# Optimization experiments

Hardware: AMD Instinct MI355X
Metric: run time of the kernel (lower is better)

The kernel has to match this reference:

```python
import jax, jax.numpy as jnp
import numpy as np

SIZE_DICT = 512
DIM_DICT = 64
TEMPERATURE = 0.5
EPS = 1e-10


def setup_inputs() -> dict:
    key = jax.random.key(0)
    k1, k2, k3 = jax.random.split(key, 3)
    bs, dz, W, H = 32, 64, 32, 32
    z = jax.random.normal(k1, (bs, dz, W, H), dtype=jnp.float32)
    var_q = jnp.ones((1,), dtype=jnp.float32)
    codebook = jax.random.normal(k2, (SIZE_DICT, DIM_DICT), dtype=jnp.float32)
    gumbel_u = jax.random.uniform(k3, (bs * W * H, SIZE_DICT), dtype=jnp.float32)
    return {"z_from_encoder": z, "var_q": var_q, "codebook": codebook, "gumbel_u": gumbel_u}


def reference(z_from_encoder, var_q, codebook, gumbel_u):
    bs, dz, W, H = z_from_encoder.shape
    # permute to channels-last and flatten: [N, D]
    z_flat = jnp.transpose(z_from_encoder, (0, 2, 3, 1)).reshape(-1, dz)
    # precision with clamping as in torch code
    precision_q = jnp.clip(1.0 / jnp.clip(var_q, 1e-5, None), None, 1e5)  # [1]
    half_prec = 0.5 * precision_q
    # squared euclidean distances to codebook: [N, K]
    dist = (jnp.sum(z_flat ** 2, axis=1, keepdims=True)
            + jnp.sum(codebook ** 2, axis=1)
            - 2.0 * z_flat @ codebook.T)
    logit = -half_prec * dist
    logit = logit - jnp.max(logit, axis=-1, keepdims=True)
    logit = jnp.clip(logit, -50.0, 50.0)
    probabilities = jax.nn.softmax(logit, axis=-1)
    log_probabilities = jax.nn.log_softmax(logit, axis=-1)
    # Gumbel-softmax sampling (training path)
    g = -jnp.log(-jnp.log(gumbel_u + EPS) + EPS)
    encodings = jax.nn.softmax((logit + g) / TEMPERATURE, axis=-1)
    # soft codebook lookup
    z_quantized = (encodings @ codebook).reshape(bs, W, H, dz)
    z_to_decoder = jnp.transpose(z_quantized, (0, 3, 1, 2))  # [bs, D, W, H]
    # discrete KLD term: sum_{n,k} p log p / bs
    kld_discrete = jnp.sum(probabilities * log_probabilities) / bs
    # continuous KLD term: mean over batch of weighted squared error
    kld_continuous = jnp.mean(
        jnp.sum((z_from_encoder - z_to_decoder) ** 2 * half_prec, axis=(1, 2, 3)))
    loss = kld_discrete + kld_continuous
    # perplexity from detached probabilities
    avg_probs = jnp.clip(jnp.mean(jax.lax.stop_gradient(probabilities), axis=0), 1e-10, None)
    perplexity = jnp.exp(-jnp.sum(avg_probs * jnp.log(avg_probs + 1e-10)))
    return z_to_decoder, loss, perplexity
```

## Files before the change

### kernel.cpp

```cpp
#include <hip/hip_runtime.h>


typedef _Float16 half8 __attribute__((ext_vector_type(8)));
typedef float f32x4 __attribute__((ext_vector_type(4)));

#define WS_B1   4096
#define WS_B2   20480
#define WS_PROB 36864
#define WS_LOSS 299008
#define WS_RED  303104
#define WS_NEED 319488

#define SMEM_PRE 24064
#define SMEM_FB  155136

__device__ __forceinline__ float half_prec(const float* var_q) {
  float vq = var_q[0];
  float pq = fminf(1.0f / fmaxf(vq, 1e-5f), 1e5f);
  return 0.5f * pq;
}

__global__ void k_pre(const float* __restrict__ var_q,
                      const float* __restrict__ cb,
                      float* __restrict__ ws, int pre) {
  int t = threadIdx.x, wg = blockIdx.x;
  if (wg == 0) {
    float hp = half_prec(var_q);
    if (t == 0) ws[512] = 0.0f;
    ws[516 + t] = 0.0f;
    const float4* row = (const float4*)(cb + t * 64);
    float s = 0.0f;
    #pragma unroll
    for (int i = 0; i < 16; ++i) {
      float4 v = row[i];
      s += v.x*v.x + v.y*v.y + v.z*v.z + v.w*v.w;
    }
    ws[t] = hp * s;
  }
  if (!pre) return;
  int gid = wg * 512 + t;
  if (gid < 4096) {
    int l = gid & 63, grp = gid >> 6;
    int tt = grp >> 1, kk = grp & 1;
    int cc = l & 15, gg = l >> 4;
    const float* src = cb + (cc*32 + tt)*64 + kk*32 + gg*8;
    float4 v0 = *(const float4*)src;
    float4 v1 = *(const float4*)(src + 4);
    half8 h = { (_Float16)v0.x, (_Float16)v0.y, (_Float16)v0.z, (_Float16)v0.w,
                (_Float16)v1.x, (_Float16)v1.y, (_Float16)v1.z, (_Float16)v1.w };
    ((half8*)(ws + WS_B1))[gid] = h;
  } else {
    int F = gid - 4096;
    int l = F & 63, grp = F >> 6;
    int kt = grp >> 2, nt = grp & 3;
    int cc = l & 15, gg = l >> 4;
    int dim = nt*16 + cc;
    half8 h;
    #pragma unroll
    for (int j = 0; j < 8; ++j) {
      int kap = gg*8 + j;
      int code = ((kap & 15) << 5) + 2*kt + (kap >> 4);
      h[j] = (_Float16)cb[code*64 + dim];
    }
    ((half8*)(ws + WS_B2))[F] = h;
  }
}

template <int PRE>
__global__ __launch_bounds__(512) void k_main_t(
    const float* __restrict__ z, const float* __restrict__ vq,
    const float* __restrict__ cb, const float* __restrict__ gu,
    float* __restrict__ out, float* __restrict__ ws)
{
  extern __shared__ char smem[];
  constexpr int CB = PRE ? 0 : 131072;
  char*  chunkAll = smem + CB;
  float* pr   = (float*)(smem + CB + 20480);
  float* redM = (float*)(smem + CB + 22528);
  float* redS = (float*)(smem + CB + 23040);
  float* redP = (float*)(smem + CB + 23552);

  const int tid  = threadIdx.x;
  const int lane = tid & 63;
  const int wv   = tid >> 6;
  const int h    = wv & 1;
  const int p    = wv >> 1;
  const int c    = lane & 15;
  const int g    = lane >> 4;

  pr[tid] = 0.0f;

  const half8* B1;
  const half8* B2;
  if constexpr (PRE) {
    B1 = (const half8*)(ws + WS_B1);
    B2 = (const half8*)(ws + WS_B2);
  } else {
    _Float16* lB1 = (_Float16*)smem;
    _Float16* lB2 = (_Float16*)(smem + 65536);
    #pragma unroll
    for (int i = 0; i < 8; ++i) {
      int F = tid + 512*i;
      int l = F & 63, grp = F >> 6;
      int t = grp >> 1, kk = grp & 1;
      int cc = l & 15, gg = l >> 4;
      const float* src = cb + (cc*32 + t)*64 + kk*32 + gg*8;
      float4 v0 = *(const float4*)src;
      float4 v1 = *(const float4*)(src + 4);
      half8 hh = { (_Float16)v0.x, (_Float16)v0.y, (_Float16)v0.z, (_Float16)v0.w,
                   (_Float16)v1.x, (_Float16)v1.y, (_Float16)v1.z, (_Float16)v1.w };
      ((half8*)lB1)[F] = hh;
    }
    #pragma unroll
    for (int i = 0; i < 8; ++i) {
      int F = tid + 512*i;
      int l = F & 63, grp = F >> 6;
      int kt = grp >> 2, nt = grp & 3;
      int cc = l & 15, gg = l >> 4;
      int dim = nt*16 + cc;
      half8 hh;
      #pragma unroll
      for (int j = 0; j < 8; ++j) {
        int kap = gg*8 + j;
        int code = ((kap & 15) << 5) + 2*kt + (kap >> 4);
        hh[j] = (_Float16)cb[code*64 + dim];
      }
      ((half8*)lB2)[F] = hh;
    }
    B1 = (const half8*)lB1;
    B2 = (const half8*)lB2;
  }

  const float hp   = half_prec(vq);
  const float s2hp = 2.0f * hp;

  const int row0 = (blockIdx.x * 4 + p) * 16;
  const int b    = row0 >> 10;
  const int wh0  = row0 & 1023;

  _Float16* zc = (_Float16*)(chunkAll + p * 5120);

  float zr[8];
  {
    const float* zp = z + ((size_t)(b*64 + lane) << 10) + wh0 + 8*h;
    float4 v0 = *(const float4*)zp;
    float4 v1 = *(const float4*)(zp + 4);
    zr[0]=v0.x; zr[1]=v0.y; zr[2]=v0.z; zr[3]=v0.w;
    zr[4]=v1.x; zr[5]=v1.y; zr[6]=v1.z; zr[7]=v1.w;
  }
  #pragma unroll
  for (int s = 0; s < 8; ++s) zc[(8*h + s)*72 + lane] = (_Float16)(zr[s] * s2hp);

  __syncthreads();

  f32x4 acc[16];
  {
    const float4* hn = (const float4*)(ws + c*32 + h*16);
    #pragma unroll
    for (int u = 0; u < 4; ++u) {
      float4 h4 = hn[u];
      acc[4*u+0] = (f32x4){-h4.x, -h4.x, -h4.x, -h4.x};
      acc[4*u+1] = (f32x4){-h4.y, -h4.y, -h4.y, -h4.y};
      acc[4*u+2] = (f32x4){-h4.z, -h4.z, -h4.z, -h4.z};
      acc[4*u+3] = (f32x4){-h4.w, -h4.w, -h4.w, -h4.w};
    }
  }

  half8 zA0 = *(const half8*)(zc + c*72 + g*8);
  half8 zA1 = *(const half8*)(zc + c*72 + 32 + g*8);

  #pragma unroll
  for (int t = 0; t < 16; ++t) {
    int tt = h*16 + t;
    acc[t] = __builtin_amdgcn_mfma_f32_16x16x32_f16(zA0, B1[(tt*2+0)*64 + lane], acc[t], 0, 0, 0);
    acc[t] = __builtin_amdgcn_mfma_f32_16x16x32_f16(zA1, B1[(tt*2+1)*64 + lane], acc[t], 0, 0, 0);
  }

  const int rix = p*32 + h*16;

  #pragma unroll
  for (int q = 0; q < 4; ++q) {
    float m = acc[0][q];
    #pragma unroll
    for (int t = 1; t < 16; ++t) m = fmaxf(m, acc[t][q]);
    #pragma unroll
    for (int o = 8; o > 0; o >>= 1) m = fmaxf(m, __shfl_xor(m, o));
    if (c == 0) redM[rix + 4*g + q] = m;
  }
  __syncthreads();
  float mq[4];
  #pragma unroll
  for (int q = 0; q < 4; ++q)
    mq[q] = fmaxf(redM[p*32 + 4*g + q], redM[p*32 + 16 + 4*g + q]);
  #pragma unroll
  for (int t = 0; t < 16; ++t)
    #pragma unroll
    for (int q = 0; q < 4; ++q) acc[t][q] -= mq[q];

  {
    float s1[4] = {0,0,0,0}, pl[4] = {0,0,0,0};
    #pragma unroll
    for (int t = 0; t < 16; ++t)
      #pragma unroll
      for (int q = 0; q < 4; ++q) {
        float e = __expf(acc[t][q]);
        s1[q] += e;
        pl[q] = fmaf(e, acc[t][q], pl[q]);
      }
    #pragma unroll
    for (int q = 0; q < 4; ++q) {
      #pragma unroll
      for (int o = 8; o > 0; o >>= 1) { s1[q] += __shfl_xor(s1[q], o); pl[q] += __shfl_xor(pl[q], o); }
      if (c == 0) { redS[rix + 4*g + q] = s1[q]; redP[rix + 4*g + q] = pl[q]; }
    }
  }
  __syncthreads();
  float kd = 0.0f, inv1[4];
  #pragma unroll
  for (int q = 0; q < 4; ++q) {
    float S = redS[p*32 + 4*g + q] + redS[p*32 + 16 + 4*g + q];
    float P = redP[p*32 + 4*g + q] + redP[p*32 + 16 + 4*g + q];
    inv1[q] = 1.0f / S;
    kd += P * inv1[q] - __logf(S);
  }

  #pragma unroll
  for (int t = 0; t < 16; ++t) {
    float v = 0.0f;
    #pragma unroll
    for (int q = 0; q < 4; ++q) v = fmaf(__expf(acc[t][q]), inv1[q], v);
    v += __shfl_xor(v, 16);
    v += __shfl_xor(v, 32);
    if (g == 0) atomicAdd(&pr[(h*16 + t)*16 + c], v);
  }

  #pragma unroll
  for (int q = 0; q < 4; ++q) {
    const float4* ub = (const float4*)(gu + ((size_t)(row0 + 4*g + q))*512 + c*32 + h*16);
    #pragma unroll
    for (int tt = 0; tt < 4; ++tt) {
      float4 u4 = ub[tt];
      float y0 = 1e-10f - __logf(u4.x + 1e-10f);
      float y1 = 1e-10f - __logf(u4.y + 1e-10f);
      float y2 = 1e-10f - __logf(u4.z + 1e-10f);
      float y3 = 1e-10f - __logf(u4.w + 1e-10f);
      acc[4*tt+0][q] = 2.0f * (acc[4*tt+0][q] - __logf(y0));
      acc[4*tt+1][q] = 2.0f * (acc[4*tt+1][q] - __logf(y1));
      acc[4*tt+2][q] = 2.0f * (acc[4*tt+2][q] - __logf(y2));
      acc[4*tt+3][q] = 2.0f * (acc[4*tt+3][q] - __logf(y3));
    }
  }

  #pragma unroll
  for (int q = 0; q < 4; ++q) {
    float m = acc[0][q];
    #pragma unroll
    for (int t = 1; t < 16; ++t) m = fmaxf(m, acc[t][q]);
    #pragma unroll
    for (int o = 8; o > 0; o >>= 1) m = fmaxf(m, __shfl_xor(m, o));
    if (c == 0) redM[rix + 4*g + q] = m;
  }
  __syncthreads();
  #pragma unroll
  for (int q = 0; q < 4; ++q) {
    float m2 = fmaxf(redM[p*32 + 4*g + q], redM[p*32 + 16 + 4*g + q]);
    float s = 0.0f;
    #pragma unroll
    for (int t = 0; t < 16; ++t) { float e = __expf(acc[t][q] - m2); acc[t][q] = e; s += e; }
    #pragma unroll
    for (int o = 8; o > 0; o >>= 1) s += __shfl_xor(s, o);
    if (c == 0) redS[rix + 4*g + q] = s;
  }
  __syncthreads();
  #pragma unroll
  for (int q = 0; q < 4; ++q) {
    float inv = 1.0f / (redS[p*32 + 4*g + q] + redS[p*32 + 16 + 4*g + q]);
    #pragma unroll
    for (int t = 0; t < 16; ++t) acc[t][q] *= inv;
  }

  f32x4 zacc[4];
  #pragma unroll
  for (int nt = 0; nt < 4; ++nt) zacc[nt] = (f32x4){0.f, 0.f, 0.f, 0.f};

  _Float16* myES = (_Float16*)(chunkAll + wv * 2560);
  #pragma unroll
  for (int k = 0; k < 8; ++k) {
    _Float16* eS = myES + (k & 1) * 640;
    #pragma unroll
    for (int tb = 0; tb < 2; ++tb)
      #pragma unroll
      for (int q = 0; q < 4; ++q)
        eS[(4*g + q)*40 + 16*tb + c] = (_Float16)acc[2*k + tb][q];
    half8 ea = *(const half8*)(eS + c*40 + g*8);
    int kt = h*8 + k;
    #pragma unroll
    for (int nt = 0; nt < 4; ++nt)
      zacc[nt] = __builtin_amdgcn_mfma_f32_16x16x32_f16(ea, B2[(kt*4 + nt)*64 + lane], zacc[nt], 0, 0, 0);
  }

  __syncthreads();
  float* zqx = (float*)chunkAll + p * 1056;
  if (h) {
    #pragma unroll
    for (int nt = 0; nt < 4; ++nt)
      #pragma unroll
      for (int q = 0; q < 4; ++q)
        zqx[(4*g + q)*66 + nt*16 + c] = zacc[nt][q];
  }
  __syncthreads();
  if (!h) {
    #pragma unroll
    for (int nt = 0; nt < 4; ++nt)
      #pragma unroll
      for (int q = 0; q < 4; ++q) {
        int ix = (4*g + q)*66 + nt*16 + c;
        zqx[ix] += zacc[nt][q];
      }
  }
  __syncthreads();

  float kc = 0.0f;
  {
    float* orow = out + ((size_t)(b*64 + lane) << 10) + wh0 + 8*h;
    float4 o0, o1;
    o0.x = zqx[(8*h + 0)*66 + lane]; o0.y = zqx[(8*h + 1)*66 + lane];
    o0.z = zqx[(8*h + 2)*66 + lane]; o0.w = zqx[(8*h + 3)*66 + lane];
    o1.x = zqx[(8*h + 4)*66 + lane]; o1.y = zqx[(8*h + 5)*66 + lane];
    o1.z = zqx[(8*h + 6)*66 + lane]; o1.w = zqx[(8*h + 7)*66 + lane];
    float d;
    d = zr[0]-o0.x; kc = fmaf(d,d,kc);  d = zr[1]-o0.y; kc = fmaf(d,d,kc);
    d = zr[2]-o0.z; kc = fmaf(d,d,kc);  d = zr[3]-o0.w; kc = fmaf(d,d,kc);
    d = zr[4]-o1.x; kc = fmaf(d,d,kc);  d = zr[5]-o1.y; kc = fmaf(d,d,kc);
    d = zr[6]-o1.z; kc = fmaf(d,d,kc);  d = zr[7]-o1.w; kc = fmaf(d,d,kc);
    *(float4*)orow       = o0;
    *(float4*)(orow + 4) = o1;
  }
  kc *= hp;

  float lv = (h ? 0.0f : kd * 0.0625f) + kc;
  #pragma unroll
  for (int o = 32; o > 0; o >>= 1) lv += __shfl_xor(lv, o);
  if (lane == 0) {
    if constexpr (PRE) ws[WS_LOSS + blockIdx.x*8 + wv] = lv;
    else               atomicAdd(&ws[512], lv);
  }

  __syncthreads();
  if constexpr (PRE) {
    ws[WS_PROB + (size_t)blockIdx.x*512 + tid] = pr[tid];
  } else {
    atomicAdd(ws + 516 + tid, pr[tid]);
  }
}

__global__ void k_red(float* __restrict__ ws) {
  int gix = blockIdx.x, t = threadIdx.x;
  float s = 0.0f;
  #pragma unroll 4
  for (int i = 0; i < 16; ++i) s += ws[WS_PROB + (size_t)(gix*16 + i)*512 + t];
  ws[WS_RED + gix*512 + t] = s;
}

__global__ void k_fin(const float* __restrict__ ws, float* __restrict__ out, int pre) {
  __shared__ float redH[16], redL[16];
  int t = threadIdx.x;
  float h = 0.0f, l = 0.0f;
  if (pre) {
    if (t < 512) {
      float s = 0.0f;
      #pragma unroll
      for (int g = 0; g < 32; ++g) s += ws[WS_RED + g*512 + t];
      float a = fmaxf(s * (1.0f/32768.0f), 1e-10f);
      h = -a * __logf(a + 1e-10f);
    } else {
      int x = t - 512;
      #pragma unroll
      for (int i = 0; i < 8; ++i) l += ws[WS_LOSS + x + 512*i];
    }
  } else {
    if (t < 512) {
      float a = fmaxf(ws[516 + t] * (1.0f/32768.0f), 1e-10f);
      h = -a * __logf(a + 1e-10f);
    } else if (t == 512) {
      l = ws[512];
    }
  }
  #pragma unroll
  for (int o = 32; o > 0; o >>= 1) { h += __shfl_xor(h, o); l += __shfl_xor(l, o); }
  if ((t & 63) == 0) { redH[t >> 6] = h; redL[t >> 6] = l; }
  __syncthreads();
  if (t == 0) {
    float H = 0.0f, L = 0.0f;
    #pragma unroll
    for (int i = 0; i < 16; ++i) { H += redH[i]; L += redL[i]; }
    out[2097152] = L * (1.0f/32.0f);
    out[2097153] = __expf(H);
  }
}

extern "C" void kernel_launch(void* const* d_in, const int* in_sizes, int n_in,
                              void* d_out, int out_size, void* d_ws, size_t ws_size,
                              hipStream_t stream) {
  const float* z  = (const float*)d_in[0];
  const float* vq = (const float*)d_in[1];
  const float* cb = (const float*)d_in[2];
  const float* gu = (const float*)d_in[3];
  float* out = (float*)d_out;
  float* ws  = (float*)d_ws;
  int pre = (ws_size >= (size_t)WS_NEED * 4) ? 1 : 0;

  hipLaunchKernelGGL(k_pre, dim3(16), dim3(512), 0, stream, vq, cb, ws, pre);
  if (pre) {
    hipLaunchKernelGGL(k_main_t<1>, dim3(512), dim3(512), SMEM_PRE, stream, z, vq, cb, gu, out, ws);
    hipLaunchKernelGGL(k_red, dim3(32), dim3(512), 0, stream, ws);
  } else {
    hipFuncSetAttribute((const void*)&k_main_t<0>, hipFuncAttributeMaxDynamicSharedMemorySize, SMEM_FB);
    hipLaunchKernelGGL(k_main_t<0>, dim3(512), dim3(512), SMEM_FB, stream, z, vq, cb, gu, out, ws);
  }
  hipLaunchKernelGGL(k_fin, dim3(1), dim3(1024), 0, stream, ws, out, pre);
}
```

Measured before the change: 68.56 us.

## Shrink main kernel blocks to one row-tile each and atomically reduce probabilities

Main kernel now uses 128-thread blocks handling one 16-row tile (2048 blocks) instead of 512-thread blocks handling four, which cuts shared memory per block and lets blocks finish independently instead of syncing four tiles together. Per-block probability partials are atomically accumulated into 512 slots (zeroed in k_pre), so k_red keeps its existing input layout. Loss partials become one per block. This adds atomic contention and more block launches, but should improve occupancy and scheduling granularity.

Measured after the change: 86.65 us. 26.4% more time.

```diff
diff --git a/kernel.cpp b/kernel.cpp
--- a/kernel.cpp
+++ b/kernel.cpp
@@ -11,8 +11,8 @@
 #define WS_RED  303104
 #define WS_NEED 319488
 
-#define SMEM_PRE 24064
-#define SMEM_FB  155136
+#define SMEM_PRE 7680
+#define SMEM_FB  138752
 
 __device__ __forceinline__ float half_prec(const float* var_q) {
   float vq = var_q[0];
@@ -24,6 +24,7 @@
                       const float* __restrict__ cb,
                       float* __restrict__ ws, int pre) {
   int t = threadIdx.x, wg = blockIdx.x;
+  int gid = wg * 512 + t;
   if (wg == 0) {
     float hp = half_prec(var_q);
     if (t == 0) ws[512] = 0.0f;
@@ -38,7 +39,8 @@
     ws[t] = hp * s;
   }
   if (!pre) return;
-  int gid = wg * 512 + t;
+  #pragma unroll
+  for (int i = 0; i < 32; ++i) ws[WS_PROB + gid + 8192*i] = 0.0f;
   if (gid < 4096) {
     int l = gid & 63, grp = gid >> 6;
     int tt = grp >> 1, kk = grp & 1;
@@ -67,28 +69,27 @@
 }
 
 template <int PRE>
-__global__ __launch_bounds__(512) void k_main_t(
+__global__ __launch_bounds__(128) void k_main_t(
     const float* __restrict__ z, const float* __restrict__ vq,
     const float* __restrict__ cb, const float* __restrict__ gu,
     float* __restrict__ out, float* __restrict__ ws)
 {
   extern __shared__ char smem[];
   constexpr int CB = PRE ? 0 : 131072;
-  char*  chunkAll = smem + CB;
-  float* pr   = (float*)(smem + CB + 20480);
-  float* redM = (float*)(smem + CB + 22528);
-  float* redS = (float*)(smem + CB + 23040);
-  float* redP = (float*)(smem + CB + 23552);
+  char*  chunk = smem + CB;
+  float* pr    = (float*)(smem + CB + 5120);
+  float* redM  = (float*)(smem + CB + 7168);
+  float* redS  = (float*)(smem + CB + 7296);
+  float* redP  = (float*)(smem + CB + 7424);
 
   const int tid  = threadIdx.x;
   const int lane = tid & 63;
-  const int wv   = tid >> 6;
-  const int h    = wv & 1;
-  const int p    = wv >> 1;
+  const int h    = tid >> 6;
   const int c    = lane & 15;
   const int g    = lane >> 4;
 
-  pr[tid] = 0.0f;
+  #pragma unroll
+  for (int i = 0; i < 4; ++i) pr[tid + 128*i] = 0.0f;
 
   const half8* B1;
   const half8* B2;
@@ -98,9 +99,8 @@
   } else {
     _Float16* lB1 = (_Float16*)smem;
     _Float16* lB2 = (_Float16*)(smem + 65536);
-    #pragma unroll
-    for (int i = 0; i < 8; ++i) {
-      int F = tid + 512*i;
+    for (int i = 0; i < 32; ++i) {
+      int F = tid + 128*i;
       int l = F & 63, grp = F >> 6;
       int t = grp >> 1, kk = grp & 1;
       int cc = l & 15, gg = l >> 4;
@@ -111,9 +111,8 @@
                    (_Float16)v1.x, (_Float16)v1.y, (_Float16)v1.z, (_Float16)v1.w };
       ((half8*)lB1)[F] = hh;
     }
-    #pragma unroll
-    for (int i = 0; i < 8; ++i) {
-      int F = tid + 512*i;
+    for (int i = 0; i < 32; ++i) {
+      int F = tid + 128*i;
       int l = F & 63, grp = F >> 6;
       int kt = grp >> 2, nt = grp & 3;
       int cc = l & 15, gg = l >> 4;
@@ -134,11 +133,11 @@
   const float hp   = half_prec(vq);
   const float s2hp = 2.0f * hp;
 
-  const int row0 = (blockIdx.x * 4 + p) * 16;
+  const int row0 = blockIdx.x * 16;
   const int b    = row0 >> 10;
   const int wh0  = row0 & 1023;
 
-  _Float16* zc = (_Float16*)(chunkAll + p * 5120);
+  _Float16* zc = (_Float16*)chunk;
 
   float zr[8];
   {
@@ -176,7 +175,7 @@
     acc[t] = __builtin_amdgcn_mfma_f32_16x16x32_f16(zA1, B1[(tt*2+1)*64 + lane], acc[t], 0, 0, 0);
   }
 
-  const int rix = p*32 + h*16;
+  const int rix = h*16;
 
   #pragma unroll
   for (int q = 0; q < 4; ++q) {
@@ -191,7 +190,7 @@
   float mq[4];
   #pragma unroll
   for (int q = 0; q < 4; ++q)
-    mq[q] = fmaxf(redM[p*32 + 4*g + q], redM[p*32 + 16 + 4*g + q]);
+    mq[q] = fmaxf(redM[4*g + q], redM[16 + 4*g + q]);
   #pragma unroll
   for (int t = 0; t < 16; ++t)
     #pragma unroll
@@ -218,8 +217,8 @@
   float kd = 0.0f, inv1[4];
   #pragma unroll
   for (int q = 0; q < 4; ++q) {
-    float S = redS[p*32 + 4*g + q] + redS[p*32 + 16 + 4*g + q];
-    float P = redP[p*32 + 4*g + q] + redP[p*32 + 16 + 4*g + q];
+    float S = redS[4*g + q] + redS[16 + 4*g + q];
+    float P = redP[4*g + q] + redP[16 + 4*g + q];
     inv1[q] = 1.0f / S;
     kd += P * inv1[q] - __logf(S);
   }
@@ -263,7 +262,7 @@
   __syncthreads();
   #pragma unroll
   for (int q = 0; q < 4; ++q) {
-    float m2 = fmaxf(redM[p*32 + 4*g + q], redM[p*32 + 16 + 4*g + q]);
+    float m2 = fmaxf(redM[4*g + q], redM[16 + 4*g + q]);
     float s = 0.0f;
     #pragma unroll
     for (int t = 0; t < 16; ++t) { float e = __expf(acc[t][q] - m2); acc[t][q] = e; s += e; }
@@ -274,7 +273,7 @@
   __syncthreads();
   #pragma unroll
   for (int q = 0; q < 4; ++q) {
-    float inv = 1.0f / (redS[p*32 + 4*g + q] + redS[p*32 + 16 + 4*g + q]);
+    float inv = 1.0f / (redS[4*g + q] + redS[16 + 4*g + q]);
     #pragma unroll
     for (int t = 0; t < 16; ++t) acc[t][q] *= inv;
   }
@@ -283,7 +282,7 @@
   #pragma unroll
   for (int nt = 0; nt < 4; ++nt) zacc[nt] = (f32x4){0.f, 0.f, 0.f, 0.f};
 
-  _Float16* myES = (_Float16*)(chunkAll + wv * 2560);
+  _Float16* myES = (_Float16*)(chunk + h * 2560);
   #pragma unroll
   for (int k = 0; k < 8; ++k) {
     _Float16* eS = myES + (k & 1) * 640;
@@ -300,7 +299,7 @@
   }
 
   __syncthreads();
-  float* zqx = (float*)chunkAll + p * 1056;
+  float* zqx = (float*)chunk;
   if (h) {
     #pragma unroll
     for (int nt = 0; nt < 4; ++nt)
@@ -341,16 +340,24 @@
   float lv = (h ? 0.0f : kd * 0.0625f) + kc;
   #pragma unroll
   for (int o = 32; o > 0; o >>= 1) lv += __shfl_xor(lv, o);
-  if (lane == 0) {
-    if constexpr (PRE) ws[WS_LOSS + blockIdx.x*8 + wv] = lv;
-    else               atomicAdd(&ws[512], lv);
-  }
-
-  __syncthreads();
+  if (lane == 0) redP[h] = lv;
+  __syncthreads();
+
   if constexpr (PRE) {
-    ws[WS_PROB + (size_t)blockIdx.x*512 + tid] = pr[tid];
+    if (tid == 0) ws[WS_LOSS + blockIdx.x] = redP[0] + redP[1];
+    int slot = blockIdx.x >> 2;
+    #pragma unroll
+    for (int i = 0; i < 4; ++i) {
+      int k = tid + 128*i;
+      atomicAdd(&ws[WS_PROB + slot*512 + k], pr[k]);
+    }
   } else {
-    atomicAdd(ws + 516 + tid, pr[tid]);
+    if (tid == 0) atomicAdd(&ws[512], redP[0] + redP[1]);
+    #pragma unroll
+    for (int i = 0; i < 4; ++i) {
+      int k = tid + 128*i;
+      atomicAdd(ws + 516 + k, pr[k]);
+    }
   }
 }
 
@@ -376,7 +383,7 @@
     } else {
       int x = t - 512;
       #pragma unroll
-      for (int i = 0; i < 8; ++i) l += ws[WS_LOSS + x + 512*i];
+      for (int i = 0; i < 4; ++i) l += ws[WS_LOSS + x + 512*i];
     }
   } else {
     if (t < 512) {
@@ -412,11 +419,11 @@
 
   hipLaunchKernelGGL(k_pre, dim3(16), dim3(512), 0, stream, vq, cb, ws, pre);
   if (pre) {
-    hipLaunchKernelGGL(k_main_t<1>, dim3(512), dim3(512), SMEM_PRE, stream, z, vq, cb, gu, out, ws);
+    hipLaunchKernelGGL(k_main_t<1>, dim3(2048), dim3(128), SMEM_PRE, stream, z, vq, cb, gu, out, ws);
     hipLaunchKernelGGL(k_red, dim3(32), dim3(512), 0, stream, ws);
   } else {
     hipFuncSetAttribute((const void*)&k_main_t<0>, hipFuncAttributeMaxDynamicSharedMemorySize, SMEM_FB);
-    hipLaunchKernelGGL(k_main_t<0>, dim3(512), dim3(512), SMEM_FB, stream, z, vq, cb, gu, out, ws);
+    hipLaunchKernelGGL(k_main_t<0>, dim3(2048), dim3(128), SMEM_FB, stream, z, vq, cb, gu, out, ws);
   }
   hipLaunchKernelGGL(k_fin, dim3(1), dim3(1024), 0, stream, ws, out, pre);
 }
```
